# Kernel optimization log

Hardware: AMD Instinct MI355X
Metric: run time of the kernel (lower is better)

## Reference

```python
import jax, jax.numpy as jnp
import numpy as np

NUM_HEADS = 16
ATTN_WINDOW = 128  # half-width; mask is |i-j| <= ATTN_WINDOW
EMBED_DIM = 1024


def setup_inputs() -> dict:
    key = jax.random.key(0)
    ks = jax.random.split(key, 9)
    B, S, D = 2, 2048, EMBED_DIM
    s = 1.0 / np.sqrt(D)
    inp = {
        "x": jax.random.normal(ks[0], (B, S, D), dtype=jnp.float32),
        "Wq": jax.random.normal(ks[1], (D, D), dtype=jnp.float32) * s,
        "bq": jnp.zeros((D,), dtype=jnp.float32),
        "Wk": jax.random.normal(ks[2], (D, D), dtype=jnp.float32) * s,
        "bk": jnp.zeros((D,), dtype=jnp.float32),
        "Wv": jax.random.normal(ks[3], (D, D), dtype=jnp.float32) * s,
        "bv": jnp.zeros((D,), dtype=jnp.float32),
        "Wo": jax.random.normal(ks[4], (D, D), dtype=jnp.float32) * s,
        "bo": jnp.zeros((D,), dtype=jnp.float32),
    }
    return inp


def reference(x, Wq, bq, Wk, bk, Wv, bv, Wo, bo):
    B, S, D = x.shape
    H = NUM_HEADS
    dh = D // H
    # projections (nn.Linear: x @ W^T + b)
    q = (x @ Wq.T + bq).reshape(B, S, H, dh).transpose(0, 2, 1, 3)  # [B,H,S,dh]
    k = (x @ Wk.T + bk).reshape(B, S, H, dh).transpose(0, 2, 1, 3)
    v = (x @ Wv.T + bv).reshape(B, S, H, dh).transpose(0, 2, 1, 3)
    scale = 1.0 / jnp.sqrt(jnp.asarray(dh, dtype=jnp.float32))
    scores = jnp.einsum("bhqd,bhkd->bhqk", q, k) * scale  # [B,H,S,S]
    # sliding-window band mask: allowed iff |i - j| <= ATTN_WINDOW
    idx = jnp.arange(S)
    band = jnp.abs(idx[:, None] - idx[None, :]) <= ATTN_WINDOW  # [S,S] bool
    scores = jnp.where(band[None, None], scores, -jnp.inf)
    attn = jax.nn.softmax(scores, axis=-1)  # each row has >=1 valid entry
    ctx = jnp.einsum("bhqk,bhkd->bhqd", attn, v)
    ctx = ctx.transpose(0, 2, 1, 3).reshape(B, S, D)
    out = ctx @ Wo.T + bo
    return out, attn
```

## Files before the change

### kernel.cpp

```cpp
#include <hip/hip_runtime.h>
#include <cstddef>

#define NB 2
#define NH 16
#define SQ 2048
#define DM 1024
#define DH 64
#define WN 128

using half8  = __attribute__((ext_vector_type(8))) _Float16;
using half4  = __attribute__((ext_vector_type(4))) _Float16;
using floatx4 = __attribute__((ext_vector_type(4))) float;

__device__ __forceinline__ void gl_lds16(const _Float16* g, _Float16* l) {
    __builtin_amdgcn_global_load_lds(
        (const __attribute__((address_space(1))) void*)g,
        (__attribute__((address_space(3))) void*)l, 16, 0, 0);
}

__global__ __launch_bounds__(256) void cvt1(const float* __restrict__ s,
                                            _Float16* __restrict__ d, int n8)
{
    int idx = blockIdx.x * 256 + threadIdx.x;
    if (idx < n8) {
        const float4 a = ((const float4*)s)[idx * 2];
        const float4 b = ((const float4*)s)[idx * 2 + 1];
        half8 h;
        h[0] = (_Float16)a.x; h[1] = (_Float16)a.y;
        h[2] = (_Float16)a.z; h[3] = (_Float16)a.w;
        h[4] = (_Float16)b.x; h[5] = (_Float16)b.y;
        h[6] = (_Float16)b.z; h[7] = (_Float16)b.w;
        ((half8*)d)[idx] = h;
    }
}

__global__ __launch_bounds__(256) void cvt4(
    const float* __restrict__ s0, const float* __restrict__ s1,
    const float* __restrict__ s2, const float* __restrict__ s3,
    _Float16* __restrict__ d0, _Float16* __restrict__ d1,
    _Float16* __restrict__ d2, _Float16* __restrict__ d3, int n8)
{
    const float* s = (blockIdx.y == 0) ? s0 : (blockIdx.y == 1) ? s1
                   : (blockIdx.y == 2) ? s2 : s3;
    _Float16*   d = (blockIdx.y == 0) ? d0 : (blockIdx.y == 1) ? d1
                   : (blockIdx.y == 2) ? d2 : d3;
    int idx = blockIdx.x * 256 + threadIdx.x;
    if (idx < n8) {
        const float4 a = ((const float4*)s)[idx * 2];
        const float4 b = ((const float4*)s)[idx * 2 + 1];
        half8 h;
        h[0] = (_Float16)a.x; h[1] = (_Float16)a.y;
        h[2] = (_Float16)a.z; h[3] = (_Float16)a.w;
        h[4] = (_Float16)b.x; h[5] = (_Float16)b.y;
        h[6] = (_Float16)b.z; h[7] = (_Float16)b.w;
        ((half8*)d)[idx] = h;
    }
}

template <int OUT_HALF>
__global__ __launch_bounds__(256) void gemm_h(
    const _Float16* __restrict__ A,
    const _Float16* __restrict__ W0, const _Float16* __restrict__ W1,
    const _Float16* __restrict__ W2,
    const float* __restrict__ b0, const float* __restrict__ b1,
    const float* __restrict__ b2,
    void* __restrict__ O0, void* __restrict__ O1, void* __restrict__ O2)
{
    constexpr int K = DM, N = DM, BK = 64;

    const _Float16* Wp = (blockIdx.z == 0) ? W0 : (blockIdx.z == 1) ? W1 : W2;
    const float*    bb = (blockIdx.z == 0) ? b0 : (blockIdx.z == 1) ? b1 : b2;
    void*           Op = (blockIdx.z == 0) ? O0 : (blockIdx.z == 1) ? O1 : O2;

    __shared__ _Float16 Asl[128 * BK];
    __shared__ _Float16 Bsl[128 * BK];

    const int tid  = threadIdx.x;
    const int lane = tid & 63;
    const int w    = tid >> 6;
    const int wm   = w & 1, wn = w >> 1;
    const int m0   = blockIdx.y * 128;
    const int n0   = blockIdx.x * 128;

    const int l8 = lane >> 3;
    const int lc = lane & 7;

    floatx4 acc[4][4];
#pragma unroll
    for (int t = 0; t < 4; ++t)
#pragma unroll
        for (int u = 0; u < 4; ++u) acc[t][u] = (floatx4){0.f, 0.f, 0.f, 0.f};

    for (int k0 = 0; k0 < K; k0 += BK) {
        __syncthreads();
#pragma unroll
        for (int i = 0; i < 4; ++i) {
            const int r  = w * 8 + l8 + i * 32;
            const int ca = lc ^ (r & 7);
            gl_lds16(A  + (size_t)(m0 + r) * K + k0 + ca * 8,
                     Asl + r * BK + lc * 8);
            gl_lds16(Wp + (size_t)(n0 + r) * K + k0 + ca * 8,
                     Bsl + r * BK + lc * 8);
        }
        __syncthreads();
#pragma unroll
        for (int kk = 0; kk < BK; kk += 32) {
            half8 af[4], bf[4];
            const int q = (kk >> 3) + (lane >> 4);
#pragma unroll
            for (int t = 0; t < 4; ++t) {
                const int ra = wm * 64 + t * 16 + (lane & 15);
                af[t] = *(const half8*)(Asl + ra * BK + ((q ^ (ra & 7)) << 3));
                const int rb = wn * 64 + t * 16 + (lane & 15);
                bf[t] = *(const half8*)(Bsl + rb * BK + ((q ^ (rb & 7)) << 3));
            }
#pragma unroll
            for (int t = 0; t < 4; ++t)
#pragma unroll
                for (int u = 0; u < 4; ++u)
                    acc[t][u] = __builtin_amdgcn_mfma_f32_16x16x32_f16(
                        af[t], bf[u], acc[t][u], 0, 0, 0);
        }
    }

    const int col0 = n0 + wn * 64 + (lane & 15);
    const int row0 = m0 + wm * 64 + ((lane >> 4) << 2);
#pragma unroll
    for (int u = 0; u < 4; ++u) {
        const int n = col0 + u * 16;
        const float bias = bb[n];
#pragma unroll
        for (int t = 0; t < 4; ++t) {
            const int m = row0 + t * 16;
#pragma unroll
            for (int r = 0; r < 4; ++r) {
                const float v = acc[t][u][r] + bias;
                if (OUT_HALF)
                    ((_Float16*)Op)[(size_t)(m + r) * N + n] = (_Float16)v;
                else
                    ((float*)Op)[(size_t)(m + r) * N + n] = v;
            }
        }
    }
}

__global__ __launch_bounds__(320) void attn_win(
    const _Float16* __restrict__ Q, const _Float16* __restrict__ K,
    const _Float16* __restrict__ V, float* __restrict__ attn,
    _Float16* __restrict__ ctx)
{
    const int tid = threadIdx.x;
    const int h = blockIdx.y, b = blockIdx.z;
    const int bh = b * NH + h;
    const int i0 = blockIdx.x * 16;
    const int wo = i0 - WN;

    __shared__ float Qs[16][DH];
    __shared__ float P[16][320];

    for (int t = tid; t < 16 * DH; t += 320) {
        const int q = t >> 6, d = t & 63;
        Qs[q][d] = (float)Q[((size_t)(b * SQ + i0 + q)) * DM + h * DH + d];
    }

    const int jg = wo + tid;
    float4 kreg[16];
    if (jg >= 0 && jg < SQ) {
        const half8* kr = (const half8*)(K + ((size_t)(b * SQ + jg)) * DM + h * DH);
#pragma unroll
        for (int d8 = 0; d8 < 8; ++d8) {
            const half8 kh = kr[d8];
            kreg[d8 * 2]     = make_float4((float)kh[0], (float)kh[1],
                                           (float)kh[2], (float)kh[3]);
            kreg[d8 * 2 + 1] = make_float4((float)kh[4], (float)kh[5],
                                           (float)kh[6], (float)kh[7]);
        }
    } else {
#pragma unroll
        for (int d4 = 0; d4 < 16; ++d4) kreg[d4] = make_float4(0.f, 0.f, 0.f, 0.f);
    }
    __syncthreads();

#pragma unroll
    for (int q = 0; q < 16; ++q) {
        const float4* q4 = (const float4*)Qs[q];
        float a0 = 0.f, a1 = 0.f, a2 = 0.f, a3 = 0.f;
#pragma unroll
        for (int d4 = 0; d4 < 16; ++d4) {
            const float4 qv = q4[d4];
            a0 = fmaf(qv.x, kreg[d4].x, a0);
            a1 = fmaf(qv.y, kreg[d4].y, a1);
            a2 = fmaf(qv.z, kreg[d4].z, a2);
            a3 = fmaf(qv.w, kreg[d4].w, a3);
        }
        const float s = ((a0 + a1) + (a2 + a3)) * 0.125f;
        const bool valid = ((unsigned)(tid - q) <= 256u) && (jg >= 0) && (jg < SQ);
        P[q][tid] = valid ? s : -1e30f;
    }
    __syncthreads();

    const int lane = tid & 63, w = tid >> 6;
    for (int q = w; q < 16; q += 5) {
        float v0 = P[q][lane],       v1 = P[q][lane + 64],
              v2 = P[q][lane + 128], v3 = P[q][lane + 192],
              v4 = P[q][lane + 256];
        float m = fmaxf(fmaxf(fmaxf(v0, v1), fmaxf(v2, v3)), v4);
        m = fmaxf(m, __shfl_xor(m, 32)); m = fmaxf(m, __shfl_xor(m, 16));
        m = fmaxf(m, __shfl_xor(m, 8));  m = fmaxf(m, __shfl_xor(m, 4));
        m = fmaxf(m, __shfl_xor(m, 2));  m = fmaxf(m, __shfl_xor(m, 1));
        float e0 = __expf(v0 - m), e1 = __expf(v1 - m), e2 = __expf(v2 - m),
              e3 = __expf(v3 - m), e4 = __expf(v4 - m);
        float sum = ((e0 + e1) + (e2 + e3)) + e4;
        sum += __shfl_xor(sum, 32); sum += __shfl_xor(sum, 16);
        sum += __shfl_xor(sum, 8);  sum += __shfl_xor(sum, 4);
        sum += __shfl_xor(sum, 2);  sum += __shfl_xor(sum, 1);
        const float inv = 1.0f / sum;
        P[q][lane]       = e0 * inv;
        P[q][lane + 64]  = e1 * inv;
        P[q][lane + 128] = e2 * inv;
        P[q][lane + 192] = e3 * inv;
        P[q][lane + 256] = e4 * inv;
    }
    __syncthreads();

    for (int idx = tid; idx < 16 * 512; idx += 320) {
        const int q  = idx >> 9;
        const int c4 = (idx & 511) << 2;
        const int jj = c4 - wo;
        float4 o;
        const unsigned u0 = (unsigned)(jj + 0 - q);
        const unsigned u1 = (unsigned)(jj + 1 - q);
        const unsigned u2 = (unsigned)(jj + 2 - q);
        const unsigned u3 = (unsigned)(jj + 3 - q);
        o.x = (u0 <= 256u) ? P[q][jj + 0] : 0.f;
        o.y = (u1 <= 256u) ? P[q][jj + 1] : 0.f;
        o.z = (u2 <= 256u) ? P[q][jj + 2] : 0.f;
        o.w = (u3 <= 256u) ? P[q][jj + 3] : 0.f;
        *(float4*)(attn + ((size_t)bh * SQ + i0 + q) * SQ + c4) = o;
    }

    const int dgrp = tid & 15, g = tid >> 4;
    if (g < 16) {
        const int q = g;
        const int d = dgrp * 4;
        const _Float16* Vrow = V + (size_t)(b * SQ) * DM + h * DH + d;
        float4 acc0 = {0,0,0,0}, acc1 = {0,0,0,0},
               acc2 = {0,0,0,0}, acc3 = {0,0,0,0};
        int j = q;
        for (; j + 4 <= q + 257; j += 4) {
            const int g0 = wo + j,     g1 = wo + j + 1,
                      g2 = wo + j + 2, g3 = wo + j + 3;
            const int c0 = g0 < 0 ? 0 : (g0 >= SQ ? SQ - 1 : g0);
            const int c1 = g1 < 0 ? 0 : (g1 >= SQ ? SQ - 1 : g1);
            const int c2 = g2 < 0 ? 0 : (g2 >= SQ ? SQ - 1 : g2);
            const int c3 = g3 < 0 ? 0 : (g3 >= SQ ? SQ - 1 : g3);
            const float p0 = P[q][j + 0], p1 = P[q][j + 1],
                        p2 = P[q][j + 2], p3 = P[q][j + 3];
            const half4 h0 = *(const half4*)(Vrow + (size_t)c0 * DM);
            const half4 h1 = *(const half4*)(Vrow + (size_t)c1 * DM);
            const half4 h2 = *(const half4*)(Vrow + (size_t)c2 * DM);
            const half4 h3 = *(const half4*)(Vrow + (size_t)c3 * DM);
            acc0.x = fmaf(p0, (float)h0[0], acc0.x); acc0.y = fmaf(p0, (float)h0[1], acc0.y);
            acc0.z = fmaf(p0, (float)h0[2], acc0.z); acc0.w = fmaf(p0, (float)h0[3], acc0.w);
            acc1.x = fmaf(p1, (float)h1[0], acc1.x); acc1.y = fmaf(p1, (float)h1[1], acc1.y);
            acc1.z = fmaf(p1, (float)h1[2], acc1.z); acc1.w = fmaf(p1, (float)h1[3], acc1.w);
            acc2.x = fmaf(p2, (float)h2[0], acc2.x); acc2.y = fmaf(p2, (float)h2[1], acc2.y);
            acc2.z = fmaf(p2, (float)h2[2], acc2.z); acc2.w = fmaf(p2, (float)h2[3], acc2.w);
            acc3.x = fmaf(p3, (float)h3[0], acc3.x); acc3.y = fmaf(p3, (float)h3[1], acc3.y);
            acc3.z = fmaf(p3, (float)h3[2], acc3.z); acc3.w = fmaf(p3, (float)h3[3], acc3.w);
        }
        {
            const int gj = wo + j;
            const int cj = gj < 0 ? 0 : (gj >= SQ ? SQ - 1 : gj);
            const float pj = P[q][j];
            const half4 hj = *(const half4*)(Vrow + (size_t)cj * DM);
            acc0.x = fmaf(pj, (float)hj[0], acc0.x); acc0.y = fmaf(pj, (float)hj[1], acc0.y);
            acc0.z = fmaf(pj, (float)hj[2], acc0.z); acc0.w = fmaf(pj, (float)hj[3], acc0.w);
        }
        half4 hv;
        hv[0] = (_Float16)((acc0.x + acc1.x) + (acc2.x + acc3.x));
        hv[1] = (_Float16)((acc0.y + acc1.y) + (acc2.y + acc3.y));
        hv[2] = (_Float16)((acc0.z + acc1.z) + (acc2.z + acc3.z));
        hv[3] = (_Float16)((acc0.w + acc1.w) + (acc2.w + acc3.w));
        *(half4*)(ctx + ((size_t)(b * SQ + i0 + q)) * DM + h * DH + d) = hv;
    }
}

extern "C" void kernel_launch(void* const* d_in, const int* in_sizes, int n_in,
                              void* d_out, int out_size, void* d_ws, size_t ws_size,
                              hipStream_t stream)
{
    const float* x  = (const float*)d_in[0];
    const float* Wq = (const float*)d_in[1];
    const float* bq = (const float*)d_in[2];
    const float* Wk = (const float*)d_in[3];
    const float* bk = (const float*)d_in[4];
    const float* Wv = (const float*)d_in[5];
    const float* bv = (const float*)d_in[6];
    const float* Wo = (const float*)d_in[7];
    const float* bo = (const float*)d_in[8];

    float* out  = (float*)d_out;
    float* attn = out + (size_t)NB * SQ * DM;

    const size_t tok = (size_t)NB * SQ * DM;
    const size_t wsz = (size_t)DM * DM;

    _Float16* xh   = (_Float16*)d_ws;
    _Float16* Wqh  = xh   + tok;
    _Float16* Wkh  = Wqh  + wsz;
    _Float16* Wvh  = Wkh  + wsz;
    _Float16* Woh  = Wvh  + wsz;
    _Float16* Qh   = Woh  + wsz;
    _Float16* Kh   = Qh   + tok;
    _Float16* Vh   = Kh   + tok;
    _Float16* ctxh = Vh   + tok;

    cvt1<<<dim3((int)(tok / 8 / 256)), dim3(256), 0, stream>>>(x, xh, (int)(tok / 8));
    cvt4<<<dim3((int)(wsz / 8 / 256), 4), dim3(256), 0, stream>>>(
        Wq, Wk, Wv, Wo, Wqh, Wkh, Wvh, Woh, (int)(wsz / 8));

    gemm_h<1><<<dim3(DM / 128, (NB * SQ) / 128, 3), dim3(256), 0, stream>>>(
        xh, Wqh, Wkh, Wvh, bq, bk, bv, Qh, Kh, Vh);

    attn_win<<<dim3(SQ / 16, NH, NB), dim3(320), 0, stream>>>(Qh, Kh, Vh, attn, ctxh);

    gemm_h<0><<<dim3(DM / 128, (NB * SQ) / 128, 1), dim3(256), 0, stream>>>(
        ctxh, Woh, Woh, Woh, bo, bo, bo, out, out, out);
}
```

Before: 791.6 us.

## Rewrite windowed attention kernel with MFMA for QK^T and PV

Replaces the scalar FP32 QK^T and PV loops in the attention kernel with 16x16x32 f16 MFMA instructions. K and Q are staged into swizzled LDS via direct global-to-LDS loads, and V is transposed into LDS. The attention-matrix write changes from full-row masked float4 stores to direct band stores plus zero-fill of the outside regions. Probabilities are rounded to fp16 before PV, which lowers precision, and the larger LDS footprint may reduce occupancy.

```diff
diff --git a/kernel.cpp b/kernel.cpp
--- a/kernel.cpp
+++ b/kernel.cpp
@@ -144,145 +144,169 @@
     }
 }
 
-__global__ __launch_bounds__(320) void attn_win(
+__global__ __launch_bounds__(256) void attn_mfma(
     const _Float16* __restrict__ Q, const _Float16* __restrict__ K,
     const _Float16* __restrict__ V, float* __restrict__ attn,
     _Float16* __restrict__ ctx)
 {
-    const int tid = threadIdx.x;
+    const int tid  = threadIdx.x;
+    const int lane = tid & 63;
+    const int w    = tid >> 6;
     const int h = blockIdx.y, b = blockIdx.z;
-    const int bh = b * NH + h;
     const int i0 = blockIdx.x * 16;
     const int wo = i0 - WN;
 
-    __shared__ float Qs[16][DH];
-    __shared__ float P[16][320];
-
-    for (int t = tid; t < 16 * DH; t += 320) {
-        const int q = t >> 6, d = t & 63;
-        Qs[q][d] = (float)Q[((size_t)(b * SQ + i0 + q)) * DM + h * DH + d];
-    }
-
-    const int jg = wo + tid;
-    float4 kreg[16];
-    if (jg >= 0 && jg < SQ) {
-        const half8* kr = (const half8*)(K + ((size_t)(b * SQ + jg)) * DM + h * DH);
-#pragma unroll
-        for (int d8 = 0; d8 < 8; ++d8) {
-            const half8 kh = kr[d8];
-            kreg[d8 * 2]     = make_float4((float)kh[0], (float)kh[1],
-                                           (float)kh[2], (float)kh[3]);
-            kreg[d8 * 2 + 1] = make_float4((float)kh[4], (float)kh[5],
-                                           (float)kh[6], (float)kh[7]);
-        }
+    __shared__ _Float16 KV[64 * 320];
+    __shared__ _Float16 Qs[16 * 64];
+    __shared__ float    Sl[16 * 276];
+    __shared__ _Float16 Pl[16 * 320];
+
+    const int l8 = lane >> 3;
+    const int lc = lane & 7;
+
+#pragma unroll
+    for (int i = 0; i < 8; ++i) {
+        const int r  = w * 8 + l8 + i * 32;
+        const int jg = wo + r;
+        const int jc = jg < 0 ? 0 : (jg >= SQ ? SQ - 1 : jg);
+        const int ca = lc ^ (r & 7);
+        gl_lds16(K + ((size_t)(b * SQ + jc)) * DM + h * DH + ca * 8,
+                 KV + r * 64 + lc * 8);
+    }
+    if (w < 2) {
+        const int r  = 256 + w * 8 + l8;
+        const int jg = wo + r;
+        const int jc = jg >= SQ ? SQ - 1 : jg;
+        const int ca = lc ^ (r & 7);
+        gl_lds16(K + ((size_t)(b * SQ + jc)) * DM + h * DH + ca * 8,
+                 KV + r * 64 + lc * 8);
     } else {
-#pragma unroll
-        for (int d4 = 0; d4 < 16; ++d4) kreg[d4] = make_float4(0.f, 0.f, 0.f, 0.f);
-    }
+        const int r  = (w - 2) * 8 + l8;
+        const int ca = lc ^ (r & 7);
+        gl_lds16(Q + ((size_t)(b * SQ + i0 + r)) * DM + h * DH + ca * 8,
+                 Qs + r * 64 + lc * 8);
+    }
+
+    half8 vr[9];
+#pragma unroll
+    for (int it = 0; it < 9; ++it) {
+        const int idx = tid + 256 * it;
+        const int j = idx >> 3, c8 = idx & 7;
+        const int jg = wo + j;
+        const int jc = jg < 0 ? 0 : (jg >= SQ ? SQ - 1 : jg);
+        vr[it] = *(const half8*)(V + ((size_t)(b * SQ + jc)) * DM + h * DH + c8 * 8);
+    }
+
     __syncthreads();
 
-#pragma unroll
-    for (int q = 0; q < 16; ++q) {
-        const float4* q4 = (const float4*)Qs[q];
-        float a0 = 0.f, a1 = 0.f, a2 = 0.f, a3 = 0.f;
-#pragma unroll
-        for (int d4 = 0; d4 < 16; ++d4) {
-            const float4 qv = q4[d4];
-            a0 = fmaf(qv.x, kreg[d4].x, a0);
-            a1 = fmaf(qv.y, kreg[d4].y, a1);
-            a2 = fmaf(qv.z, kreg[d4].z, a2);
-            a3 = fmaf(qv.w, kreg[d4].w, a3);
-        }
-        const float s = ((a0 + a1) + (a2 + a3)) * 0.125f;
-        const bool valid = ((unsigned)(tid - q) <= 256u) && (jg >= 0) && (jg < SQ);
-        P[q][tid] = valid ? s : -1e30f;
+    half8 af0, af1;
+    {
+        const int row = lane & 15;
+        af0 = *(const half8*)(Qs + row * 64 + ((((lane >> 4))     ^ (row & 7)) << 3));
+        af1 = *(const half8*)(Qs + row * 64 + (((4 + (lane >> 4)) ^ (row & 7)) << 3));
+    }
+    for (int t = w; t < 17; t += 4) {
+        const int rb = t * 16 + (lane & 15);
+        half8 bf0 = *(const half8*)(KV + rb * 64 + ((((lane >> 4))     ^ (rb & 7)) << 3));
+        half8 bf1 = *(const half8*)(KV + rb * 64 + (((4 + (lane >> 4)) ^ (rb & 7)) << 3));
+        floatx4 acc = (floatx4){0.f, 0.f, 0.f, 0.f};
+        acc = __builtin_amdgcn_mfma_f32_16x16x32_f16(af0, bf0, acc, 0, 0, 0);
+        acc = __builtin_amdgcn_mfma_f32_16x16x32_f16(af1, bf1, acc, 0, 0, 0);
+        const int jloc = t * 16 + (lane & 15);
+        const int jg   = wo + jloc;
+        const bool inr = (jg >= 0) && (jg < SQ);
+#pragma unroll
+        for (int r = 0; r < 4; ++r) {
+            const int q = ((lane >> 4) << 2) + r;
+            const bool valid = ((unsigned)(jloc - q) <= 256u) && inr;
+            Sl[q * 276 + jloc] = valid ? acc[r] * 0.125f : -1e30f;
+        }
     }
     __syncthreads();
 
-    const int lane = tid & 63, w = tid >> 6;
-    for (int q = w; q < 16; q += 5) {
-        float v0 = P[q][lane],       v1 = P[q][lane + 64],
-              v2 = P[q][lane + 128], v3 = P[q][lane + 192],
-              v4 = P[q][lane + 256];
+#pragma unroll
+    for (int it = 0; it < 9; ++it) {
+        const int idx = tid + 256 * it;
+        const int j = idx >> 3, c8 = idx & 7;
+        const int jc3 = j >> 3, jl = j & 7;
+#pragma unroll
+        for (int e = 0; e < 8; ++e) {
+            const int d = c8 * 8 + e;
+            KV[d * 320 + ((jc3 ^ ((c8 + e) & 7)) << 3) + jl] = vr[it][e];
+        }
+    }
+
+    for (int q = w; q < 16; q += 4) {
+        const float* Srow = Sl + q * 276;
+        const float v0 = Srow[lane];
+        const float v1 = Srow[lane + 64];
+        const float v2 = Srow[lane + 128];
+        const float v3 = Srow[lane + 192];
+        const float v4 = (lane < 16) ? Srow[lane + 256] : -1e30f;
         float m = fmaxf(fmaxf(fmaxf(v0, v1), fmaxf(v2, v3)), v4);
-        m = fmaxf(m, __shfl_xor(m, 32)); m = fmaxf(m, __shfl_xor(m, 16));
-        m = fmaxf(m, __shfl_xor(m, 8));  m = fmaxf(m, __shfl_xor(m, 4));
-        m = fmaxf(m, __shfl_xor(m, 2));  m = fmaxf(m, __shfl_xor(m, 1));
+        m = fmaxf(m, __shfl_xor(m, 32));
+        m = fmaxf(m, __shfl_xor(m, 16));
+        m = fmaxf(m, __shfl_xor(m, 8));
+        m = fmaxf(m, __shfl_xor(m, 4));
+        m = fmaxf(m, __shfl_xor(m, 2));
+        m = fmaxf(m, __shfl_xor(m, 1));
         float e0 = __expf(v0 - m), e1 = __expf(v1 - m), e2 = __expf(v2 - m),
               e3 = __expf(v3 - m), e4 = __expf(v4 - m);
-        float sum = ((e0 + e1) + (e2 + e3)) + e4;
-        sum += __shfl_xor(sum, 32); sum += __shfl_xor(sum, 16);
-        sum += __shfl_xor(sum, 8);  sum += __shfl_xor(sum, 4);
-        sum += __shfl_xor(sum, 2);  sum += __shfl_xor(sum, 1);
-        const float inv = 1.0f / sum;
-        P[q][lane]       = e0 * inv;
-        P[q][lane + 64]  = e1 * inv;
-        P[q][lane + 128] = e2 * inv;
-        P[q][lane + 192] = e3 * inv;
-        P[q][lane + 256] = e4 * inv;
+        float s = ((e0 + e1) + (e2 + e3)) + e4;
+        s += __shfl_xor(s, 32); s += __shfl_xor(s, 16); s += __shfl_xor(s, 8);
+        s += __shfl_xor(s, 4);  s += __shfl_xor(s, 2);  s += __shfl_xor(s, 1);
+        const float inv = 1.0f / s;
+        e0 *= inv; e1 *= inv; e2 *= inv; e3 *= inv; e4 *= inv;
+
+        const int fq = (q + (q >> 3)) & 7;
+        _Float16* Prow = Pl + q * 320;
+        Prow[((((lane      ) >> 3) ^ fq) << 3) + (lane & 7)] = (_Float16)e0;
+        Prow[((((lane +  64) >> 3) ^ fq) << 3) + (lane & 7)] = (_Float16)e1;
+        Prow[((((lane + 128) >> 3) ^ fq) << 3) + (lane & 7)] = (_Float16)e2;
+        Prow[((((lane + 192) >> 3) ^ fq) << 3) + (lane & 7)] = (_Float16)e3;
+        if (lane < 16) {
+            Prow[((((lane + 256) >> 3) ^ fq) << 3) + (lane & 7)] = (_Float16)e4;
+            Prow[((((lane + 272) >> 3) ^ fq) << 3) + (lane & 7)] = (_Float16)0.f;
+        }
+
+        float* arow = attn + ((size_t)(b * NH + h) * SQ + i0 + q) * SQ;
+        const int g0 = wo + lane;
+        if ((unsigned)(g0      ) < (unsigned)SQ) arow[g0      ] = e0;
+        if ((unsigned)(g0 +  64) < (unsigned)SQ) arow[g0 +  64] = e1;
+        if ((unsigned)(g0 + 128) < (unsigned)SQ) arow[g0 + 128] = e2;
+        if ((unsigned)(g0 + 192) < (unsigned)SQ) arow[g0 + 192] = e3;
+        if (lane < 16 && (unsigned)(g0 + 256) < (unsigned)SQ) arow[g0 + 256] = e4;
+        const int a0 = wo > 0 ? wo : 0;
+        const int b0 = (wo + 272 < SQ) ? (wo + 272) : SQ;
+        const float4 z4 = make_float4(0.f, 0.f, 0.f, 0.f);
+        float4* za = (float4*)arow;
+        const int na = a0 >> 2;
+        for (int c = lane; c < na; c += 64) za[c] = z4;
+        float4* zb = (float4*)(arow + b0);
+        const int nb = (SQ - b0) >> 2;
+        for (int c = lane; c < nb; c += 64) zb[c] = z4;
     }
     __syncthreads();
 
-    for (int idx = tid; idx < 16 * 512; idx += 320) {
-        const int q  = idx >> 9;
-        const int c4 = (idx & 511) << 2;
-        const int jj = c4 - wo;
-        float4 o;
-        const unsigned u0 = (unsigned)(jj + 0 - q);
-        const unsigned u1 = (unsigned)(jj + 1 - q);
-        const unsigned u2 = (unsigned)(jj + 2 - q);
-        const unsigned u3 = (unsigned)(jj + 3 - q);
-        o.x = (u0 <= 256u) ? P[q][jj + 0] : 0.f;
-        o.y = (u1 <= 256u) ? P[q][jj + 1] : 0.f;
-        o.z = (u2 <= 256u) ? P[q][jj + 2] : 0.f;
-        o.w = (u3 <= 256u) ? P[q][jj + 3] : 0.f;
-        *(float4*)(attn + ((size_t)bh * SQ + i0 + q) * SQ + c4) = o;
-    }
-
-    const int dgrp = tid & 15, g = tid >> 4;
-    if (g < 16) {
-        const int q = g;
-        const int d = dgrp * 4;
-        const _Float16* Vrow = V + (size_t)(b * SQ) * DM + h * DH + d;
-        float4 acc0 = {0,0,0,0}, acc1 = {0,0,0,0},
-               acc2 = {0,0,0,0}, acc3 = {0,0,0,0};
-        int j = q;
-        for (; j + 4 <= q + 257; j += 4) {
-            const int g0 = wo + j,     g1 = wo + j + 1,
-                      g2 = wo + j + 2, g3 = wo + j + 3;
-            const int c0 = g0 < 0 ? 0 : (g0 >= SQ ? SQ - 1 : g0);
-            const int c1 = g1 < 0 ? 0 : (g1 >= SQ ? SQ - 1 : g1);
-            const int c2 = g2 < 0 ? 0 : (g2 >= SQ ? SQ - 1 : g2);
-            const int c3 = g3 < 0 ? 0 : (g3 >= SQ ? SQ - 1 : g3);
-            const float p0 = P[q][j + 0], p1 = P[q][j + 1],
-                        p2 = P[q][j + 2], p3 = P[q][j + 3];
-            const half4 h0 = *(const half4*)(Vrow + (size_t)c0 * DM);
-            const half4 h1 = *(const half4*)(Vrow + (size_t)c1 * DM);
-            const half4 h2 = *(const half4*)(Vrow + (size_t)c2 * DM);
-            const half4 h3 = *(const half4*)(Vrow + (size_t)c3 * DM);
-            acc0.x = fmaf(p0, (float)h0[0], acc0.x); acc0.y = fmaf(p0, (float)h0[1], acc0.y);
-            acc0.z = fmaf(p0, (float)h0[2], acc0.z); acc0.w = fmaf(p0, (float)h0[3], acc0.w);
-            acc1.x = fmaf(p1, (float)h1[0], acc1.x); acc1.y = fmaf(p1, (float)h1[1], acc1.y);
-            acc1.z = fmaf(p1, (float)h1[2], acc1.z); acc1.w = fmaf(p1, (float)h1[3], acc1.w);
-            acc2.x = fmaf(p2, (float)h2[0], acc2.x); acc2.y = fmaf(p2, (float)h2[1], acc2.y);
-            acc2.z = fmaf(p2, (float)h2[2], acc2.z); acc2.w = fmaf(p2, (float)h2[3], acc2.w);
-            acc3.x = fmaf(p3, (float)h3[0], acc3.x); acc3.y = fmaf(p3, (float)h3[1], acc3.y);
-            acc3.z = fmaf(p3, (float)h3[2], acc3.z); acc3.w = fmaf(p3, (float)h3[3], acc3.w);
-        }
-        {
-            const int gj = wo + j;
-            const int cj = gj < 0 ? 0 : (gj >= SQ ? SQ - 1 : gj);
-            const float pj = P[q][j];
-            const half4 hj = *(const half4*)(Vrow + (size_t)cj * DM);
-            acc0.x = fmaf(pj, (float)hj[0], acc0.x); acc0.y = fmaf(pj, (float)hj[1], acc0.y);
-            acc0.z = fmaf(pj, (float)hj[2], acc0.z); acc0.w = fmaf(pj, (float)hj[3], acc0.w);
-        }
-        half4 hv;
-        hv[0] = (_Float16)((acc0.x + acc1.x) + (acc2.x + acc3.x));
-        hv[1] = (_Float16)((acc0.y + acc1.y) + (acc2.y + acc3.y));
-        hv[2] = (_Float16)((acc0.z + acc1.z) + (acc2.z + acc3.z));
-        hv[3] = (_Float16)((acc0.w + acc1.w) + (acc2.w + acc3.w));
-        *(half4*)(ctx + ((size_t)(b * SQ + i0 + q)) * DM + h * DH + d) = hv;
+    {
+        const int rowp = lane & 15;
+        const int fp = (rowp + (rowp >> 3)) & 7;
+        const int rowv = w * 16 + (lane & 15);
+        const int fv = (rowv + (rowv >> 3)) & 7;
+        floatx4 acc = (floatx4){0.f, 0.f, 0.f, 0.f};
+#pragma unroll
+        for (int ks = 0; ks < 9; ++ks) {
+            const int lch = ks * 4 + (lane >> 4);
+            half8 ap = *(const half8*)(Pl + rowp * 320 + ((lch ^ fp) << 3));
+            half8 bp = *(const half8*)(KV + rowv * 320 + ((lch ^ fv) << 3));
+            acc = __builtin_amdgcn_mfma_f32_16x16x32_f16(ap, bp, acc, 0, 0, 0);
+        }
+        const int dcol = w * 16 + (lane & 15);
+#pragma unroll
+        for (int r = 0; r < 4; ++r) {
+            const int q = ((lane >> 4) << 2) + r;
+            ctx[((size_t)(b * SQ + i0 + q)) * DM + h * DH + dcol] = (_Float16)acc[r];
+        }
     }
 }
 
@@ -323,7 +347,7 @@
     gemm_h<1><<<dim3(DM / 128, (NB * SQ) / 128, 3), dim3(256), 0, stream>>>(
         xh, Wqh, Wkh, Wvh, bq, bk, bv, Qh, Kh, Vh);
 
-    attn_win<<<dim3(SQ / 16, NH, NB), dim3(320), 0, stream>>>(Qh, Kh, Vh, attn, ctxh);
+    attn_mfma<<<dim3(SQ / 16, NH, NB), dim3(256), 0, stream>>>(Qh, Kh, Vh, attn, ctxh);
 
     gemm_h<0><<<dim3(DM / 128, (NB * SQ) / 128, 1), dim3(256), 0, stream>>>(
         ctxh, Woh, Woh, Woh, bo, bo, bo, out, out, out);
```

Result: faster. 660.9 us (-16.5%).
